# Performance work log

Hardware: AMD Instinct MI355X
Metric: run time of the kernel (lower is better)

Reference implementation:

```python
import jax, jax.numpy as jnp
import numpy as np

N, D, C, P = 256, 1024, 4, 46  # nodes, embedding_dim, max children, num dependency labels
NEG = -1e30  # masked-out candidate value for the max-reduce


def setup_inputs() -> dict:
    key = jax.random.key(0)
    k1, k2 = jax.random.split(key)
    embeddings = jax.random.normal(k1, (N, D), dtype=jnp.float32)
    # Xavier-uniform init of the per-dependency [D,D] matrices, as in _init_params
    scale = float(np.sqrt(6.0 / (D + D)))
    params = jax.random.uniform(k2, (P, D, D), dtype=jnp.float32, minval=-scale, maxval=scale)
    # Build a random tree in topological order: children of node i have index < i;
    # node N-1 is the root. Padded child slots are masked out.
    rng = np.random.default_rng(0)
    c_idx = np.zeros((N, C), dtype=np.int32)
    c_mask = np.zeros((N, C), dtype=bool)
    for i in range(1, N):
        n_children = int(rng.integers(0, C + 1))  # 0 => leaf-like internal node
        c_idx[i] = rng.integers(0, i, size=C)
        c_mask[i, :n_children] = True
    c_mask[N - 1, :] = True  # root always has children
    c_dep = rng.integers(0, P, size=(N, C)).astype(np.int32)
    return {
        "embeddings": embeddings,
        "params": params,
        "children_idx": jnp.asarray(c_idx),
        "children_dep": jnp.asarray(c_dep),
        "children_mask": jnp.asarray(c_mask),
    }


def reference(embeddings, params, children_idx, children_dep, children_mask):
    """Tree-structured dependency encoder.

    For each node i (children first, topological order):
      leaf:     z_i = x_i
      internal: cand_c = params[dep_c] * relu(z_child_c)[None, :]   # [D, D] per child
                mult   = max over children of cand_c                 # [D, D]
                z_i    = x_i @ mult                                  # [D]
    Returns the root embedding, shape [1, D] (matches torch output).
    """
    n_nodes, d = embeddings.shape

    def step(z, inp):
        i, c_idx, c_dep, c_mask = inp
        child_z = jax.nn.relu(z[c_idx])                      # [C, D]
        cand = params[c_dep] * child_z[:, None, :]           # [C, D, D]
        cand = jnp.where(c_mask[:, None, None], cand, NEG)
        mult = jnp.max(cand, axis=0)                         # [D, D]
        x = embeddings[i]                                    # [D]
        z_i = jnp.where(jnp.any(c_mask), x @ mult, x)
        return z.at[i].set(z_i), None

    z0 = jnp.zeros_like(embeddings)
    idxs = jnp.arange(n_nodes)
    z, _ = jax.lax.scan(step, z0, (idxs, children_idx, children_dep, children_mask))
    return z[-1:]  # root node is last in topological order -> [1, D]
```

## Files before the change

kernel.cpp:

```cpp
#include <hip/hip_runtime.h>
#include <cstddef>

#define NN 256
#define DD 1024
#define CC 4
#define NT 512
#define ROOT (NN - 1)


struct St {
  float4 p0, p1;
  float x0, x1;
};

__device__ __forceinline__ float4 relu4(float4 v) {
  float4 r;
  r.x = fmaxf(v.x, 0.f); r.y = fmaxf(v.y, 0.f);
  r.z = fmaxf(v.z, 0.f); r.w = fmaxf(v.w, 0.f);
  return r;
}
__device__ __forceinline__ float4 mul4(float4 a, float4 b) {
  float4 r; r.x = a.x*b.x; r.y = a.y*b.y; r.z = a.z*b.z; r.w = a.w*b.w; return r;
}
__device__ __forceinline__ float4 max4(float4 a, float4 b) {
  float4 r;
  r.x = fmaxf(a.x, b.x); r.y = fmaxf(a.y, b.y);
  r.z = fmaxf(a.z, b.z); r.w = fmaxf(a.w, b.w);
  return r;
}
__device__ __forceinline__ void fma4(float4& acc, float4 m, float s) {
  acc.x = fmaf(m.x, s, acc.x); acc.y = fmaf(m.y, s, acc.y);
  acc.z = fmaf(m.z, s, acc.z); acc.w = fmaf(m.w, s, acc.w);
}

__device__ __forceinline__ void ld_stage(St& S, int e, const float* __restrict__ par,
                                         const float* __restrict__ emb,
                                         const short* e_meta, const short* e_node,
                                         int j0, int r2) {
  const int meta = e_meta[e];
  const int dep = meta & 0x3FFF;
  const float* pb = par + (((size_t)dep) << 20) + (((size_t)r2) << 10) + j0;
  S.p0 = *(const float4*)(pb);
  S.p1 = *(const float4*)(pb + DD);
  if (meta & 0x8000) {
    const float2 xx = *(const float2*)(emb + (((size_t)e_node[e]) << 10) + r2);
    S.x0 = xx.x; S.x1 = xx.y;
  }
}

__device__ __forceinline__ void cmp_stage(const St& S, int e, float4& m0, float4& m1,
                                          float (*z_loc)[4], float (*s_part)[4],
                                          const short* e_child, const short* e_meta,
                                          const short* e_node, int tid) {
  const int meta = e_meta[e];
  const float4 u = relu4(*(const float4*)z_loc[e_child[e]]);
  if (meta & 0x4000) {
    m0 = mul4(S.p0, u);
    m1 = mul4(S.p1, u);
  } else {
    m0 = max4(m0, mul4(S.p0, u));
    m1 = max4(m1, mul4(S.p1, u));
  }
  if (meta & 0x8000) {
    float4 acc = {0.f, 0.f, 0.f, 0.f};
    fma4(acc, m0, S.x0);
    fma4(acc, m1, S.x1);
#pragma unroll
    for (int off = 1; off < 64; off <<= 1) {
      acc.x += __shfl_xor(acc.x, off, 64);
      acc.y += __shfl_xor(acc.y, off, 64);
      acc.z += __shfl_xor(acc.z, off, 64);
      acc.w += __shfl_xor(acc.w, off, 64);
    }
    if ((tid & 63) == 0) *(float4*)s_part[tid >> 6] = acc;
    __syncthreads();
    if (tid < 4) {
      float s = 0.f;
#pragma unroll
      for (int k = 0; k < 8; ++k) s += s_part[k][tid];
      z_loc[e_node[e]][tid] = s;
    }
    __syncthreads();
  }
}

__global__ __launch_bounds__(NT, 1) void dep_col_kernel(
    const float* __restrict__ emb, const float* __restrict__ par,
    const int* __restrict__ cidx, const int* __restrict__ cdep,
    const unsigned char* __restrict__ cmask, float* __restrict__ out) {
  __shared__ float z_loc[NN][4];
  __shared__ short s_ci[NN][CC];
  __shared__ short s_cd[NN][CC];
  __shared__ short s_nc[NN];
  __shared__ int s_pfx[NN];
  __shared__ unsigned char s_reach[NN];
  __shared__ short s_e_child[NN * CC];
  __shared__ short s_e_meta[NN * CC];
  __shared__ short s_e_node[NN * CC];
  __shared__ int s_NE;
  __shared__ int s_flag;
  __shared__ float s_part[8][4];

  const int tid = threadIdx.x;
  const int strip = blockIdx.x & 63;
  const int quad = blockIdx.x >> 6;
  const int j0 = strip * 16 + quad * 4;
  const int r2 = tid << 1;

  if (tid == 0)
    s_flag = (cmask[1021] == 1 && cmask[1022] == 1 && cmask[1023] == 1);
  __syncthreads();
  const bool m_u8 = (s_flag != 0);
  const int* m32 = (const int*)cmask;
  if (tid < NN) {
    int nc = 0;
#pragma unroll
    for (int c = 0; c < CC; ++c) {
      bool mk = m_u8 ? (cmask[tid * CC + c] != 0) : (m32[tid * CC + c] != 0);
      if (mk) {
        s_ci[tid][nc] = (short)cidx[tid * CC + c];
        s_cd[tid][nc] = (short)cdep[tid * CC + c];
        ++nc;
      }
    }
    s_nc[tid] = (short)nc;
    s_reach[tid] = (tid == ROOT) ? 1 : 0;
  }
  __syncthreads();

  for (int it = 0; it < NN + 2; ++it) {
    if (tid == 0) s_flag = 0;
    __syncthreads();
    if (tid < NN && s_reach[tid] && s_nc[tid] > 0) {
      for (int c = 0; c < s_nc[tid]; ++c) {
        const int ch = s_ci[tid][c];
        if (!s_reach[ch]) { s_reach[ch] = 1; s_flag = 1; }
      }
    }
    __syncthreads();
    const int chg = s_flag;
    __syncthreads();
    if (!chg) break;
  }

  const int wgt = (tid < NN && s_reach[tid] && s_nc[tid] > 0) ? (int)s_nc[tid] : 0;
  if (tid < NN) s_pfx[tid] = wgt;
  __syncthreads();
  for (int off = 1; off < NN; off <<= 1) {
    int v = 0;
    if (tid < NN && tid >= off) v = s_pfx[tid - off];
    __syncthreads();
    if (tid < NN) s_pfx[tid] += v;
    __syncthreads();
  }
  if (tid < NN && wgt > 0) {
    const int st = s_pfx[tid] - wgt;
    for (int c = 0; c < wgt; ++c) {
      s_e_child[st + c] = s_ci[tid][c];
      int meta = (int)s_cd[tid][c];
      if (c == 0) meta |= 1 << 14;
      if (c == wgt - 1) meta |= 1 << 15;
      s_e_meta[st + c] = (short)meta;
      s_e_node[st + c] = (short)tid;
    }
  }
  if (tid == NN - 1) s_NE = s_pfx[NN - 1];

  if (tid < NN) {
    const float4 e = *(const float4*)(emb + (((size_t)tid) << 10) + j0);
    *(float4*)z_loc[tid] = e;
  }
  __syncthreads();
  const int NE = s_NE;

  St A, B, C, D;
  float4 m0, m1;
  if (NE > 0) ld_stage(A, 0, par, emb, s_e_meta, s_e_node, j0, r2);
  if (NE > 1) ld_stage(B, 1, par, emb, s_e_meta, s_e_node, j0, r2);
  if (NE > 2) ld_stage(C, 2, par, emb, s_e_meta, s_e_node, j0, r2);
  int e = 0;
  while (e < NE) {
    if (e + 3 < NE) ld_stage(D, e + 3, par, emb, s_e_meta, s_e_node, j0, r2);
    cmp_stage(A, e, m0, m1, z_loc, s_part, s_e_child, s_e_meta, s_e_node, tid);
    if (++e >= NE) break;
    if (e + 3 < NE) ld_stage(A, e + 3, par, emb, s_e_meta, s_e_node, j0, r2);
    cmp_stage(B, e, m0, m1, z_loc, s_part, s_e_child, s_e_meta, s_e_node, tid);
    if (++e >= NE) break;
    if (e + 3 < NE) ld_stage(B, e + 3, par, emb, s_e_meta, s_e_node, j0, r2);
    cmp_stage(C, e, m0, m1, z_loc, s_part, s_e_child, s_e_meta, s_e_node, tid);
    if (++e >= NE) break;
    if (e + 3 < NE) ld_stage(C, e + 3, par, emb, s_e_meta, s_e_node, j0, r2);
    cmp_stage(D, e, m0, m1, z_loc, s_part, s_e_child, s_e_meta, s_e_node, tid);
    ++e;
  }

  if (tid < 4) out[j0 + tid] = z_loc[ROOT][tid];
}

extern "C" void kernel_launch(void* const* d_in, const int* in_sizes, int n_in,
                              void* d_out, int out_size, void* d_ws, size_t ws_size,
                              hipStream_t stream) {
  const float* emb = (const float*)d_in[0];
  const float* par = (const float*)d_in[1];
  const int* cidx = (const int*)d_in[2];
  const int* cdep = (const int*)d_in[3];
  const unsigned char* cmask = (const unsigned char*)d_in[4];
  float* out = (float*)d_out;

  hipLaunchKernelGGL(dep_col_kernel, dim3(256), dim3(NT), 0, stream, emb, par,
                     cidx, cdep, cmask, out);
}
```

Before: 124.7 us.

## Cut per-node barriers with double-buffered partials, register-forwarded child z, deeper prefetch

Each node's final reduction now uses one barrier instead of two. Partial sums are double-buffered in shared memory, and every thread redundantly sums the eight wave partials instead of only four threads doing it. The previous active node's result is kept in a register, and a prefix-max scan flags children that equal it so their value skips the shared-memory read. The parameter prefetch pipeline deepens from 4 to 6 stages, and the root output is written from the register. This removes serial barrier latency on the dependency chain at the cost of more registers and a narrower 13-bit dep field.

```diff
diff --git a/kernel.cpp b/kernel.cpp
--- a/kernel.cpp
+++ b/kernel.cpp
@@ -28,17 +28,13 @@
   r.z = fmaxf(a.z, b.z); r.w = fmaxf(a.w, b.w);
   return r;
 }
-__device__ __forceinline__ void fma4(float4& acc, float4 m, float s) {
-  acc.x = fmaf(m.x, s, acc.x); acc.y = fmaf(m.y, s, acc.y);
-  acc.z = fmaf(m.z, s, acc.z); acc.w = fmaf(m.w, s, acc.w);
-}
 
 __device__ __forceinline__ void ld_stage(St& S, int e, const float* __restrict__ par,
                                          const float* __restrict__ emb,
                                          const short* e_meta, const short* e_node,
                                          int j0, int r2) {
   const int meta = e_meta[e];
-  const int dep = meta & 0x3FFF;
+  const int dep = meta & 0x1FFF;
   const float* pb = par + (((size_t)dep) << 20) + (((size_t)r2) << 10) + j0;
   S.p0 = *(const float4*)(pb);
   S.p1 = *(const float4*)(pb + DD);
@@ -49,12 +45,16 @@
 }
 
 __device__ __forceinline__ void cmp_stage(const St& S, int e, float4& m0, float4& m1,
-                                          float (*z_loc)[4], float (*s_part)[4],
+                                          float4& zreg, int& par,
+                                          float (*z_loc)[4], float s_part[2][8][4],
                                           const short* e_child, const short* e_meta,
                                           const short* e_node, int tid) {
   const int meta = e_meta[e];
-  const float4 u = relu4(*(const float4*)z_loc[e_child[e]]);
-  if (meta & 0x4000) {
+  float4 zc;
+  if (meta & (1 << 13)) zc = zreg;
+  else zc = *(const float4*)z_loc[e_child[e]];
+  const float4 u = relu4(zc);
+  if (meta & (1 << 14)) {
     m0 = mul4(S.p0, u);
     m1 = mul4(S.p1, u);
   } else {
@@ -62,9 +62,11 @@
     m1 = max4(m1, mul4(S.p1, u));
   }
   if (meta & 0x8000) {
-    float4 acc = {0.f, 0.f, 0.f, 0.f};
-    fma4(acc, m0, S.x0);
-    fma4(acc, m1, S.x1);
+    float4 acc;
+    acc.x = fmaf(S.x1, m1.x, S.x0 * m0.x);
+    acc.y = fmaf(S.x1, m1.y, S.x0 * m0.y);
+    acc.z = fmaf(S.x1, m1.z, S.x0 * m0.z);
+    acc.w = fmaf(S.x1, m1.w, S.x0 * m0.w);
 #pragma unroll
     for (int off = 1; off < 64; off <<= 1) {
       acc.x += __shfl_xor(acc.x, off, 64);
@@ -72,20 +74,26 @@
       acc.z += __shfl_xor(acc.z, off, 64);
       acc.w += __shfl_xor(acc.w, off, 64);
     }
-    if ((tid & 63) == 0) *(float4*)s_part[tid >> 6] = acc;
-    __syncthreads();
-    if (tid < 4) {
-      float s = 0.f;
+    if ((tid & 63) == 0) *(float4*)s_part[par][tid >> 6] = acc;
+    asm volatile("s_waitcnt lgkmcnt(0)" ::: "memory");
+    __builtin_amdgcn_s_barrier();
+    __builtin_amdgcn_sched_barrier(0);
+    float4 s4 = {0.f, 0.f, 0.f, 0.f};
 #pragma unroll
-      for (int k = 0; k < 8; ++k) s += s_part[k][tid];
-      z_loc[e_node[e]][tid] = s;
-    }
-    __syncthreads();
+    for (int k = 0; k < 8; ++k) {
+      s4.x += s_part[par][k][0];
+      s4.y += s_part[par][k][1];
+      s4.z += s_part[par][k][2];
+      s4.w += s_part[par][k][3];
+    }
+    zreg = s4;
+    if (tid == 0) *(float4*)z_loc[e_node[e]] = s4;
+    par ^= 1;
   }
 }
 
 __global__ __launch_bounds__(NT, 1) void dep_col_kernel(
-    const float* __restrict__ emb, const float* __restrict__ par,
+    const float* __restrict__ emb, const float* __restrict__ par_,
     const int* __restrict__ cidx, const int* __restrict__ cdep,
     const unsigned char* __restrict__ cmask, float* __restrict__ out) {
   __shared__ float z_loc[NN][4];
@@ -93,13 +101,14 @@
   __shared__ short s_cd[NN][CC];
   __shared__ short s_nc[NN];
   __shared__ int s_pfx[NN];
+  __shared__ int s_mx[NN];
   __shared__ unsigned char s_reach[NN];
   __shared__ short s_e_child[NN * CC];
   __shared__ short s_e_meta[NN * CC];
   __shared__ short s_e_node[NN * CC];
   __shared__ int s_NE;
   __shared__ int s_flag;
-  __shared__ float s_part[8][4];
+  __shared__ float s_part[2][8][4];
 
   const int tid = threadIdx.x;
   const int strip = blockIdx.x & 63;
@@ -143,21 +152,31 @@
     if (!chg) break;
   }
 
-  const int wgt = (tid < NN && s_reach[tid] && s_nc[tid] > 0) ? (int)s_nc[tid] : 0;
-  if (tid < NN) s_pfx[tid] = wgt;
+  const int activ = (tid < NN && s_reach[tid] && s_nc[tid] > 0) ? 1 : 0;
+  const int wgt = activ ? (int)s_nc[tid] : 0;
+  if (tid < NN) {
+    s_pfx[tid] = wgt;
+    s_mx[tid] = activ ? tid : -1;
+  }
   __syncthreads();
   for (int off = 1; off < NN; off <<= 1) {
-    int v = 0;
-    if (tid < NN && tid >= off) v = s_pfx[tid - off];
-    __syncthreads();
-    if (tid < NN) s_pfx[tid] += v;
-    __syncthreads();
-  }
-  if (tid < NN && wgt > 0) {
+    int v = 0, w = -1;
+    if (tid < NN && tid >= off) { v = s_pfx[tid - off]; w = s_mx[tid - off]; }
+    __syncthreads();
+    if (tid < NN) {
+      s_pfx[tid] += v;
+      s_mx[tid] = max(s_mx[tid], w);
+    }
+    __syncthreads();
+  }
+  if (activ) {
+    const int prv = (tid > 0) ? s_mx[tid - 1] : -1;
     const int st = s_pfx[tid] - wgt;
     for (int c = 0; c < wgt; ++c) {
-      s_e_child[st + c] = s_ci[tid][c];
+      const int ch = s_ci[tid][c];
+      s_e_child[st + c] = (short)ch;
       int meta = (int)s_cd[tid][c];
+      if (ch == prv) meta |= 1 << 13;
       if (c == 0) meta |= 1 << 14;
       if (c == wgt - 1) meta |= 1 << 15;
       s_e_meta[st + c] = (short)meta;
@@ -173,28 +192,38 @@
   __syncthreads();
   const int NE = s_NE;
 
-  St A, B, C, D;
+  St A, B, C, D, E, F;
   float4 m0, m1;
-  if (NE > 0) ld_stage(A, 0, par, emb, s_e_meta, s_e_node, j0, r2);
-  if (NE > 1) ld_stage(B, 1, par, emb, s_e_meta, s_e_node, j0, r2);
-  if (NE > 2) ld_stage(C, 2, par, emb, s_e_meta, s_e_node, j0, r2);
+  float4 zreg = {0.f, 0.f, 0.f, 0.f};
+  int par = 0;
+  if (NE > 0) ld_stage(A, 0, par_, emb, s_e_meta, s_e_node, j0, r2);
+  if (NE > 1) ld_stage(B, 1, par_, emb, s_e_meta, s_e_node, j0, r2);
+  if (NE > 2) ld_stage(C, 2, par_, emb, s_e_meta, s_e_node, j0, r2);
+  if (NE > 3) ld_stage(D, 3, par_, emb, s_e_meta, s_e_node, j0, r2);
+  if (NE > 4) ld_stage(E, 4, par_, emb, s_e_meta, s_e_node, j0, r2);
   int e = 0;
   while (e < NE) {
-    if (e + 3 < NE) ld_stage(D, e + 3, par, emb, s_e_meta, s_e_node, j0, r2);
-    cmp_stage(A, e, m0, m1, z_loc, s_part, s_e_child, s_e_meta, s_e_node, tid);
-    if (++e >= NE) break;
-    if (e + 3 < NE) ld_stage(A, e + 3, par, emb, s_e_meta, s_e_node, j0, r2);
-    cmp_stage(B, e, m0, m1, z_loc, s_part, s_e_child, s_e_meta, s_e_node, tid);
-    if (++e >= NE) break;
-    if (e + 3 < NE) ld_stage(B, e + 3, par, emb, s_e_meta, s_e_node, j0, r2);
-    cmp_stage(C, e, m0, m1, z_loc, s_part, s_e_child, s_e_meta, s_e_node, tid);
-    if (++e >= NE) break;
-    if (e + 3 < NE) ld_stage(C, e + 3, par, emb, s_e_meta, s_e_node, j0, r2);
-    cmp_stage(D, e, m0, m1, z_loc, s_part, s_e_child, s_e_meta, s_e_node, tid);
+    if (e + 5 < NE) ld_stage(F, e + 5, par_, emb, s_e_meta, s_e_node, j0, r2);
+    cmp_stage(A, e, m0, m1, zreg, par, z_loc, s_part, s_e_child, s_e_meta, s_e_node, tid);
+    if (++e >= NE) break;
+    if (e + 5 < NE) ld_stage(A, e + 5, par_, emb, s_e_meta, s_e_node, j0, r2);
+    cmp_stage(B, e, m0, m1, zreg, par, z_loc, s_part, s_e_child, s_e_meta, s_e_node, tid);
+    if (++e >= NE) break;
+    if (e + 5 < NE) ld_stage(B, e + 5, par_, emb, s_e_meta, s_e_node, j0, r2);
+    cmp_stage(C, e, m0, m1, zreg, par, z_loc, s_part, s_e_child, s_e_meta, s_e_node, tid);
+    if (++e >= NE) break;
+    if (e + 5 < NE) ld_stage(C, e + 5, par_, emb, s_e_meta, s_e_node, j0, r2);
+    cmp_stage(D, e, m0, m1, zreg, par, z_loc, s_part, s_e_child, s_e_meta, s_e_node, tid);
+    if (++e >= NE) break;
+    if (e + 5 < NE) ld_stage(D, e + 5, par_, emb, s_e_meta, s_e_node, j0, r2);
+    cmp_stage(E, e, m0, m1, zreg, par, z_loc, s_part, s_e_child, s_e_meta, s_e_node, tid);
+    if (++e >= NE) break;
+    if (e + 5 < NE) ld_stage(E, e + 5, par_, emb, s_e_meta, s_e_node, j0, r2);
+    cmp_stage(F, e, m0, m1, zreg, par, z_loc, s_part, s_e_child, s_e_meta, s_e_node, tid);
     ++e;
   }
 
-  if (tid < 4) out[j0 + tid] = z_loc[ROOT][tid];
+  if (tid == 0) *(float4*)(out + j0) = zreg;
 }
 
 extern "C" void kernel_launch(void* const* d_in, const int* in_sizes, int n_in,
```

Measured after the change: 135.8 us. 1.09x slower.

## Pre-transpose parameter matrices so each block reads contiguous column rows

Applied to the files above, without the earlier changes.

Adds a kernel that transposes all 46 DxD parameter matrices into a global device buffer. The tree-walk kernel then reads each output column's parameters as contiguous float2 rows instead of strided float4 pieces. The aim is better memory coalescing in the walk, which is bound by memory latency. The cost is a full read and write of the ~190MB parameter tensor on every call, which is likely far more traffic than the walk itself uses.

```diff
diff --git a/kernel.cpp b/kernel.cpp
--- a/kernel.cpp
+++ b/kernel.cpp
@@ -4,12 +4,45 @@
 #define NN 256
 #define DD 1024
 #define CC 4
+#define NP 46
 #define NT 512
 #define ROOT (NN - 1)
 
+__device__ float g_Pt[NP][DD][DD];
+
+__global__ __launch_bounds__(256) void transpose_kernel(
+    const float* __restrict__ par) {
+  const int b = blockIdx.x;
+  const int p = b >> 6;
+  const int t = b & 63;
+  const int tr = (t >> 3) << 7;
+  const int tc = (t & 7) << 7;
+  const int tid = threadIdx.x;
+  const float* src = par + ((size_t)p << 20);
+  float* dst = &g_Pt[p][0][0];
+  const int mc = tid & 31;
+#pragma unroll
+  for (int k = 0; k < 4; ++k) {
+    const int mr = (tid >> 5) + (k << 3);
+    const int r4 = tr + (mr << 2);
+    const int c4 = tc + (mc << 2);
+    const float4 v0 = *(const float4*)(src + (size_t)(r4 + 0) * DD + c4);
+    const float4 v1 = *(const float4*)(src + (size_t)(r4 + 1) * DD + c4);
+    const float4 v2 = *(const float4*)(src + (size_t)(r4 + 2) * DD + c4);
+    const float4 v3 = *(const float4*)(src + (size_t)(r4 + 3) * DD + c4);
+    const float4 w0 = {v0.x, v1.x, v2.x, v3.x};
+    const float4 w1 = {v0.y, v1.y, v2.y, v3.y};
+    const float4 w2 = {v0.z, v1.z, v2.z, v3.z};
+    const float4 w3 = {v0.w, v1.w, v2.w, v3.w};
+    *(float4*)(dst + (size_t)(c4 + 0) * DD + r4) = w0;
+    *(float4*)(dst + (size_t)(c4 + 1) * DD + r4) = w1;
+    *(float4*)(dst + (size_t)(c4 + 2) * DD + r4) = w2;
+    *(float4*)(dst + (size_t)(c4 + 3) * DD + r4) = w3;
+  }
+}
 
 struct St {
-  float4 p0, p1;
+  float2 p0, p1, p2, p3;
   float x0, x1;
 };
 
@@ -19,52 +52,51 @@
   r.z = fmaxf(v.z, 0.f); r.w = fmaxf(v.w, 0.f);
   return r;
 }
-__device__ __forceinline__ float4 mul4(float4 a, float4 b) {
-  float4 r; r.x = a.x*b.x; r.y = a.y*b.y; r.z = a.z*b.z; r.w = a.w*b.w; return r;
-}
-__device__ __forceinline__ float4 max4(float4 a, float4 b) {
-  float4 r;
-  r.x = fmaxf(a.x, b.x); r.y = fmaxf(a.y, b.y);
-  r.z = fmaxf(a.z, b.z); r.w = fmaxf(a.w, b.w);
-  return r;
-}
-__device__ __forceinline__ void fma4(float4& acc, float4 m, float s) {
-  acc.x = fmaf(m.x, s, acc.x); acc.y = fmaf(m.y, s, acc.y);
-  acc.z = fmaf(m.z, s, acc.z); acc.w = fmaf(m.w, s, acc.w);
-}
-
-__device__ __forceinline__ void ld_stage(St& S, int e, const float* __restrict__ par,
+
+__device__ __forceinline__ void ld_stage(St& S, int e, const float* __restrict__ pt,
                                          const float* __restrict__ emb,
                                          const short* e_meta, const short* e_node,
                                          int j0, int r2) {
   const int meta = e_meta[e];
-  const int dep = meta & 0x3FFF;
-  const float* pb = par + (((size_t)dep) << 20) + (((size_t)r2) << 10) + j0;
-  S.p0 = *(const float4*)(pb);
-  S.p1 = *(const float4*)(pb + DD);
+  const int dep = meta & 0x1FFF;
+  const float* pb = pt + (((size_t)dep) << 20) + (((size_t)j0) << 10) + r2;
+  S.p0 = *(const float2*)(pb);
+  S.p1 = *(const float2*)(pb + DD);
+  S.p2 = *(const float2*)(pb + 2 * DD);
+  S.p3 = *(const float2*)(pb + 3 * DD);
   if (meta & 0x8000) {
     const float2 xx = *(const float2*)(emb + (((size_t)e_node[e]) << 10) + r2);
     S.x0 = xx.x; S.x1 = xx.y;
   }
 }
 
-__device__ __forceinline__ void cmp_stage(const St& S, int e, float4& m0, float4& m1,
+__device__ __forceinline__ float2 mul2s(float2 a, float s) {
+  float2 r; r.x = a.x * s; r.y = a.y * s; return r;
+}
+__device__ __forceinline__ float2 max2(float2 a, float2 b) {
+  float2 r; r.x = fmaxf(a.x, b.x); r.y = fmaxf(a.y, b.y); return r;
+}
+
+__device__ __forceinline__ void cmp_stage(const St& S, int e, float2& m0, float2& m1,
+                                          float2& m2, float2& m3,
                                           float (*z_loc)[4], float (*s_part)[4],
                                           const short* e_child, const short* e_meta,
                                           const short* e_node, int tid) {
   const int meta = e_meta[e];
   const float4 u = relu4(*(const float4*)z_loc[e_child[e]]);
-  if (meta & 0x4000) {
-    m0 = mul4(S.p0, u);
-    m1 = mul4(S.p1, u);
+  if (meta & (1 << 14)) {
+    m0 = mul2s(S.p0, u.x); m1 = mul2s(S.p1, u.y);
+    m2 = mul2s(S.p2, u.z); m3 = mul2s(S.p3, u.w);
   } else {
-    m0 = max4(m0, mul4(S.p0, u));
-    m1 = max4(m1, mul4(S.p1, u));
+    m0 = max2(m0, mul2s(S.p0, u.x)); m1 = max2(m1, mul2s(S.p1, u.y));
+    m2 = max2(m2, mul2s(S.p2, u.z)); m3 = max2(m3, mul2s(S.p3, u.w));
   }
   if (meta & 0x8000) {
-    float4 acc = {0.f, 0.f, 0.f, 0.f};
-    fma4(acc, m0, S.x0);
-    fma4(acc, m1, S.x1);
+    float4 acc;
+    acc.x = fmaf(S.x1, m0.y, S.x0 * m0.x);
+    acc.y = fmaf(S.x1, m1.y, S.x0 * m1.x);
+    acc.z = fmaf(S.x1, m2.y, S.x0 * m2.x);
+    acc.w = fmaf(S.x1, m3.y, S.x0 * m3.x);
 #pragma unroll
     for (int off = 1; off < 64; off <<= 1) {
       acc.x += __shfl_xor(acc.x, off, 64);
@@ -84,10 +116,10 @@
   }
 }
 
-__global__ __launch_bounds__(NT, 1) void dep_col_kernel(
-    const float* __restrict__ emb, const float* __restrict__ par,
-    const int* __restrict__ cidx, const int* __restrict__ cdep,
-    const unsigned char* __restrict__ cmask, float* __restrict__ out) {
+__global__ __launch_bounds__(NT, 1) void walk_kernel(
+    const float* __restrict__ emb, const int* __restrict__ cidx,
+    const int* __restrict__ cdep, const unsigned char* __restrict__ cmask,
+    float* __restrict__ out) {
   __shared__ float z_loc[NN][4];
   __shared__ short s_ci[NN][CC];
   __shared__ short s_cd[NN][CC];
@@ -102,10 +134,9 @@
   __shared__ float s_part[8][4];
 
   const int tid = threadIdx.x;
-  const int strip = blockIdx.x & 63;
-  const int quad = blockIdx.x >> 6;
-  const int j0 = strip * 16 + quad * 4;
+  const int j0 = blockIdx.x << 2;
   const int r2 = tid << 1;
+  const float* pt = &g_Pt[0][0][0];
 
   if (tid == 0)
     s_flag = (cmask[1021] == 1 && cmask[1022] == 1 && cmask[1023] == 1);
@@ -174,23 +205,23 @@
   const int NE = s_NE;
 
   St A, B, C, D;
-  float4 m0, m1;
-  if (NE > 0) ld_stage(A, 0, par, emb, s_e_meta, s_e_node, j0, r2);
-  if (NE > 1) ld_stage(B, 1, par, emb, s_e_meta, s_e_node, j0, r2);
-  if (NE > 2) ld_stage(C, 2, par, emb, s_e_meta, s_e_node, j0, r2);
+  float2 m0, m1, m2, m3;
+  if (NE > 0) ld_stage(A, 0, pt, emb, s_e_meta, s_e_node, j0, r2);
+  if (NE > 1) ld_stage(B, 1, pt, emb, s_e_meta, s_e_node, j0, r2);
+  if (NE > 2) ld_stage(C, 2, pt, emb, s_e_meta, s_e_node, j0, r2);
   int e = 0;
   while (e < NE) {
-    if (e + 3 < NE) ld_stage(D, e + 3, par, emb, s_e_meta, s_e_node, j0, r2);
-    cmp_stage(A, e, m0, m1, z_loc, s_part, s_e_child, s_e_meta, s_e_node, tid);
+    if (e + 3 < NE) ld_stage(D, e + 3, pt, emb, s_e_meta, s_e_node, j0, r2);
+    cmp_stage(A, e, m0, m1, m2, m3, z_loc, s_part, s_e_child, s_e_meta, s_e_node, tid);
     if (++e >= NE) break;
-    if (e + 3 < NE) ld_stage(A, e + 3, par, emb, s_e_meta, s_e_node, j0, r2);
-    cmp_stage(B, e, m0, m1, z_loc, s_part, s_e_child, s_e_meta, s_e_node, tid);
+    if (e + 3 < NE) ld_stage(A, e + 3, pt, emb, s_e_meta, s_e_node, j0, r2);
+    cmp_stage(B, e, m0, m1, m2, m3, z_loc, s_part, s_e_child, s_e_meta, s_e_node, tid);
     if (++e >= NE) break;
-    if (e + 3 < NE) ld_stage(B, e + 3, par, emb, s_e_meta, s_e_node, j0, r2);
-    cmp_stage(C, e, m0, m1, z_loc, s_part, s_e_child, s_e_meta, s_e_node, tid);
+    if (e + 3 < NE) ld_stage(B, e + 3, pt, emb, s_e_meta, s_e_node, j0, r2);
+    cmp_stage(C, e, m0, m1, m2, m3, z_loc, s_part, s_e_child, s_e_meta, s_e_node, tid);
     if (++e >= NE) break;
-    if (e + 3 < NE) ld_stage(C, e + 3, par, emb, s_e_meta, s_e_node, j0, r2);
-    cmp_stage(D, e, m0, m1, z_loc, s_part, s_e_child, s_e_meta, s_e_node, tid);
+    if (e + 3 < NE) ld_stage(C, e + 3, pt, emb, s_e_meta, s_e_node, j0, r2);
+    cmp_stage(D, e, m0, m1, m2, m3, z_loc, s_part, s_e_child, s_e_meta, s_e_node, tid);
     ++e;
   }
 
@@ -207,6 +238,7 @@
   const unsigned char* cmask = (const unsigned char*)d_in[4];
   float* out = (float*)d_out;
 
-  hipLaunchKernelGGL(dep_col_kernel, dim3(256), dim3(NT), 0, stream, emb, par,
-                     cidx, cdep, cmask, out);
-}
+  hipLaunchKernelGGL(transpose_kernel, dim3(NP * 64), dim3(256), 0, stream, par);
+  hipLaunchKernelGGL(walk_kernel, dim3(256), dim3(NT), 0, stream, emb, cidx,
+                     cdep, cmask, out);
+}
```

Measured after the change: 176.5 us. 41.6% more time.
